# Performance work log

Measured on AMD Instinct MI355X. Metric: run time of the kernel, lower is better.

The kernel has to match this reference:

```python
import jax, jax.numpy as jnp
import numpy as np

N_EMBED = 1024
HEAD_SIZE = 128

def setup_inputs() -> dict:
    key = jax.random.key(0)
    kx, kq, kk, kv = jax.random.split(key, 4)
    B, T = 8, 2048
    x = jax.random.normal(kx, (B, T, N_EMBED), dtype=jnp.float32)
    s = 1.0 / np.sqrt(N_EMBED)
    Wq = jax.random.normal(kq, (N_EMBED, HEAD_SIZE), dtype=jnp.float32) * s
    Wk = jax.random.normal(kk, (N_EMBED, HEAD_SIZE), dtype=jnp.float32) * s
    Wv = jax.random.normal(kv, (N_EMBED, HEAD_SIZE), dtype=jnp.float32) * s
    return {"x": x, "Wq": Wq, "Wk": Wk, "Wv": Wv}

def reference(x, Wq, Wk, Wv):
    # x: [B, T, E]; single-head causal attention (nanoGPT-style Head)
    B, T, E = x.shape
    q = jnp.einsum('bte,eh->bth', x, Wq)  # [B,T,H]
    k = jnp.einsum('bte,eh->bth', x, Wk)
    v = jnp.einsum('bte,eh->bth', x, Wv)
    scale = 1.0 / jnp.sqrt(jnp.asarray(q.shape[-1], dtype=x.dtype))
    wei = jnp.einsum('bqh,bkh->bqk', q, k) * scale  # [B,T,T]
    causal = jnp.tril(jnp.ones((T, T), dtype=bool))
    wei = jnp.where(causal[None, :, :], wei, jnp.asarray(-jnp.inf, dtype=wei.dtype))
    attn = jax.nn.softmax(wei, axis=-1)
    out = jnp.einsum('bqk,bkh->bqh', attn, v)  # [B,T,H]
    return out
```

## Files before the change

### kernel.cpp

```cpp
#include <hip/hip_runtime.h>
#include <hip/hip_bf16.h>

typedef __bf16 bf16_t;
typedef bf16_t bf16x8 __attribute__((ext_vector_type(8)));
typedef bf16_t bf16x4 __attribute__((ext_vector_type(4)));
typedef float f32x4 __attribute__((ext_vector_type(4)));

#define MFMA16(a, b, c) __builtin_amdgcn_mfma_f32_16x16x32_bf16((a), (b), (c), 0, 0, 0)

#define TT 2048
#define EE 1024
#define HH 128
#define UPB 288


__global__ __launch_bounds__(256) void prep_w_kernel(
    const float* __restrict__ Wq, const float* __restrict__ Wk,
    const float* __restrict__ Wv, bf16_t* __restrict__ Wf)
{
    int idx = blockIdx.x * 256 + threadIdx.x;
    int e  = idx & 7;
    int c  = (idx >> 3) & 15;
    int g  = (idx >> 7) & 3;
    int kt = (idx >> 9) & 31;
    int ct = idx >> 14;
    int w  = ct >> 3;
    const float* W = (w == 0) ? Wq : (w == 1) ? Wk : Wv;
    int k = kt * 32 + g * 8 + e;
    int n = (ct & 7) * 16 + c;
    Wf[idx] = (bf16_t)W[k * HH + n];
}

__global__ __launch_bounds__(256) void qkv_kernel(
    const float* __restrict__ x, const bf16_t* __restrict__ Wf,
    bf16_t* __restrict__ Qf, bf16_t* __restrict__ Kf, bf16_t* __restrict__ Vf)
{
    __shared__ __attribute__((aligned(16))) bf16_t As[2][32][72];
    const int row0 = blockIdx.x * 32;
    const int tid  = threadIdx.x;
    const int lane = tid & 63;
    const int wn   = tid >> 6;
    const int g = lane >> 4, c = lane & 15;

    const int srow0 = tid >> 4;
    const int srow1 = 16 + srow0;
    const int scg   = (tid & 15) * 4;
    const float* xp0 = x + (size_t)(row0 + srow0) * EE + scg;
    const float* xp1 = x + (size_t)(row0 + srow1) * EE + scg;

    const bf16_t* wfbase = Wf + (size_t)wn * 6 * 32 * 512 + lane * 8;

    f32x4 acc[2][6];
    for (int i = 0; i < 2; ++i)
        for (int j = 0; j < 6; ++j) acc[i][j] = (f32x4)0.0f;

    f32x4 f0[2], f1[2];
    bf16x8 w[2][12];

#define BAR() do {                                                            \
    asm volatile("s_waitcnt lgkmcnt(0)" ::: "memory");                        \
    __builtin_amdgcn_s_barrier();                                             \
    __builtin_amdgcn_sched_barrier(0);                                        \
} while (0)
#define XLOAD(S, T) do {                                                      \
    f0[S] = *(const f32x4*)(xp0 + (size_t)(T) * 64);                          \
    f1[S] = *(const f32x4*)(xp1 + (size_t)(T) * 64);                          \
} while (0)
#define WLOAD(S, T) do {                                                      \
    for (int kk = 0; kk < 2; ++kk)                                            \
        for (int nt = 0; nt < 6; ++nt)                                        \
            w[S][kk * 6 + nt] = *(const bf16x8*)(wfbase +                     \
                ((size_t)nt * 32 + (T) * 2 + kk) * 512);                      \
} while (0)
#define XWRITE(S, BUF) do {                                                   \
    union { bf16_t h[4]; unsigned long long u; } p0_, p1_;                    \
    p0_.h[0] = (bf16_t)f0[S][0]; p0_.h[1] = (bf16_t)f0[S][1];                 \
    p0_.h[2] = (bf16_t)f0[S][2]; p0_.h[3] = (bf16_t)f0[S][3];                 \
    p1_.h[0] = (bf16_t)f1[S][0]; p1_.h[1] = (bf16_t)f1[S][1];                 \
    p1_.h[2] = (bf16_t)f1[S][2]; p1_.h[3] = (bf16_t)f1[S][3];                 \
    *reinterpret_cast<unsigned long long*>(&As[BUF][srow0][scg]) = p0_.u;     \
    *reinterpret_cast<unsigned long long*>(&As[BUF][srow1][scg]) = p1_.u;     \
} while (0)
#define PHASE(CUR, OTH, T) do {                                               \
    if ((T) + 2 < 16) XLOAD(CUR, (T) + 2);                                    \
    for (int kk = 0; kk < 2; ++kk)                                            \
        for (int mt = 0; mt < 2; ++mt) {                                      \
            bf16x8 af = *(const bf16x8*)&As[CUR][mt * 16 + c][kk * 32 + g * 8]; \
            for (int nt = 0; nt < 6; ++nt)                                    \
                acc[mt][nt] = MFMA16(af, w[CUR][kk * 6 + nt], acc[mt][nt]);   \
        }                                                                     \
    if ((T) + 2 < 16) WLOAD(CUR, (T) + 2);                                    \
    if ((T) + 1 < 16) XWRITE(OTH, OTH);                                       \
    BAR();                                                                    \
} while (0)

    XLOAD(0, 0);
    XLOAD(1, 1);
    WLOAD(0, 0);
    WLOAD(1, 1);
    XWRITE(0, 0);
    BAR();

    for (int tt = 0; tt < 16; tt += 2) {
        PHASE(0, 1, tt);
        PHASE(1, 0, tt + 1);
    }
#undef PHASE
#undef XLOAD
#undef WLOAD
#undef XWRITE
#undef BAR

    const float sc = 0.08838834764831845f * 1.4426950408889634f;
    for (int mt = 0; mt < 2; ++mt)
        for (int nt = 0; nt < 6; ++nt) {
            int cb = wn * 96 + nt * 16;
            int w_ = cb >> 7;
            int hl = (cb & 127) + c;
            int t0 = row0 + mt * 16 + g * 4;
            if (w_ == 2) {
                int b  = t0 >> 11;
                int ttr = t0 & (TT - 1);
                int vc = ttr >> 5, gg = (ttr & 31) >> 3, j0 = ttr & 7;
                int hb = hl >> 4, cc = hl & 15;
                union { bf16_t h4[4]; unsigned long long u; } pk;
                for (int i = 0; i < 4; ++i) pk.h4[i] = (bf16_t)acc[mt][nt][i];
                *reinterpret_cast<unsigned long long*>(
                    Vf + ((size_t)((b * 64 + vc) * 8 + hb)) * 512 +
                    (gg * 16 + cc) * 8 + j0) = pk.u;
            } else {
                bf16_t* dst = (w_ == 0) ? Qf : Kf;
                float s = (w_ == 0) ? sc : 1.0f;
                int kk = hl >> 5, gg = (hl & 31) >> 3, e = hl & 7;
                int grt = t0 >> 4;
                for (int i = 0; i < 4; ++i) {
                    int cr = (t0 + i) & 15;
                    dst[((size_t)(grt * 4 + kk)) * 512 + (gg * 16 + cr) * 8 + e] =
                        (bf16_t)(acc[mt][nt][i] * s);
                }
            }
        }
}

__global__ __launch_bounds__(256) void attn_kernel(
    const bf16_t* __restrict__ Qf, const bf16_t* __restrict__ Kf,
    const bf16_t* __restrict__ Vf, bf16_t* __restrict__ Pacc,
    float* __restrict__ Pml)
{
    __shared__ __attribute__((aligned(16))) bf16_t Pl[4][32][40];
    const int tid = threadIdx.x, lane = tid & 63, wid = tid >> 6;
    const int g = lane >> 4, c = lane & 15;
    bf16_t (*P)[40] = Pl[wid];

    const int bx = blockIdx.x;
    const int b  = bx & 7;
    const int u  = 287 - ((bx >> 3) * 4 + wid);
    int k = 0;
    while (4 * (k + 1) * (k + 2) <= u) ++k;
    const int r  = u - 4 * k * (k + 1);
    const int qt = 8 * k + r / (k + 1);
    const int ch = r - (r / (k + 1)) * (k + 1);
    const int q0 = qt * 32;
    const int kv_lo = ch * 256;
    int kv_hi = kv_lo + 256; if (kv_hi > q0 + 32) kv_hi = q0 + 32;
    const int sid = b * UPB + 4 * k * (k + 1) + (qt & 7) * (k + 1) + ch;

    bf16x8 qA[4], qB[4];
    for (int kk = 0; kk < 4; ++kk) {
        qA[kk] = *(const bf16x8*)(Qf +
            ((size_t)((b * 128 + (q0 >> 4)) * 4 + kk)) * 512 + lane * 8);
        qB[kk] = *(const bf16x8*)(Qf +
            ((size_t)((b * 128 + (q0 >> 4) + 1) * 4 + kk)) * 512 + lane * 8);
    }

    f32x4 accA[8], accB[8];
    for (int hb = 0; hb < 8; ++hb) { accA[hb] = (f32x4)0.0f; accB[hb] = (f32x4)0.0f; }
    float lsA[4] = {0, 0, 0, 0}, lsB[4] = {0, 0, 0, 0};

    for (int kv0 = kv_lo; kv0 < kv_hi; kv0 += 32) {
        const int kt = b * 128 + (kv0 >> 4);
        bf16x8 k0f[4], k1f[4], vf[8];
        for (int kk = 0; kk < 4; ++kk) {
            k0f[kk] = *(const bf16x8*)(Kf + ((size_t)(kt * 4 + kk)) * 512 + lane * 8);
            k1f[kk] = *(const bf16x8*)(Kf + ((size_t)((kt + 1) * 4 + kk)) * 512 + lane * 8);
        }
        const int vcb = (b * 64 + (kv0 >> 5)) * 8;
        for (int hb = 0; hb < 8; ++hb)
            vf[hb] = *(const bf16x8*)(Vf + ((size_t)(vcb + hb)) * 512 + lane * 8);

        f32x4 sA0 = (f32x4)0.0f, sA1 = (f32x4)0.0f;
        f32x4 sB0 = (f32x4)0.0f, sB1 = (f32x4)0.0f;
        for (int kk = 0; kk < 4; ++kk) {
            sA0 = MFMA16(qA[kk], k0f[kk], sA0);
            sA1 = MFMA16(qA[kk], k1f[kk], sA1);
            sB0 = MFMA16(qB[kk], k0f[kk], sB0);
            sB1 = MFMA16(qB[kk], k1f[kk], sB1);
        }
        if (kv0 + 32 > q0) {
            for (int i = 0; i < 4; ++i) {
                int row = q0 + g * 4 + i;
                if (kv0 + c > row)      sA0[i] = -1e30f;
                if (kv0 + 16 + c > row) sA1[i] = -1e30f;
            }
        }
        if (kv0 + 32 > q0 + 16) {
            for (int i = 0; i < 4; ++i) {
                int row = q0 + 16 + g * 4 + i;
                if (kv0 + c > row)      sB0[i] = -1e30f;
                if (kv0 + 16 + c > row) sB1[i] = -1e30f;
            }
        }
        float pA0[4], pA1[4], pB0[4], pB1[4];
        for (int i = 0; i < 4; ++i) {
            pA0[i] = exp2f(sA0[i]); pA1[i] = exp2f(sA1[i]);
            pB0[i] = exp2f(sB0[i]); pB1[i] = exp2f(sB1[i]);
            lsA[i] += pA0[i] + pA1[i];
            lsB[i] += pB0[i] + pB1[i];
        }
        for (int i = 0; i < 4; ++i) {
            P[g * 4 + i][c]           = (bf16_t)pA0[i];
            P[g * 4 + i][c + 16]      = (bf16_t)pA1[i];
            P[16 + g * 4 + i][c]      = (bf16_t)pB0[i];
            P[16 + g * 4 + i][c + 16] = (bf16_t)pB1[i];
        }
        __builtin_amdgcn_wave_barrier();
        asm volatile("s_waitcnt lgkmcnt(0)" ::: "memory");
        __builtin_amdgcn_sched_barrier(0);
        bf16x8 paA = *(const bf16x8*)&P[c][g * 8];
        bf16x8 paB = *(const bf16x8*)&P[16 + c][g * 8];
        __builtin_amdgcn_s_setprio(1);
        for (int hb = 0; hb < 8; ++hb) {
            accA[hb] = MFMA16(paA, vf[hb], accA[hb]);
            accB[hb] = MFMA16(paB, vf[hb], accB[hb]);
        }
        __builtin_amdgcn_s_setprio(0);
        __builtin_amdgcn_wave_barrier();
    }

    for (int off = 1; off < 16; off <<= 1)
        for (int i = 0; i < 4; ++i) {
            lsA[i] += __shfl_xor(lsA[i], off, 64);
            lsB[i] += __shfl_xor(lsB[i], off, 64);
        }
    if (c == 0)
        for (int i = 0; i < 4; ++i) {
            Pml[(size_t)sid * 32 + g * 4 + i]      = lsA[i];
            Pml[(size_t)sid * 32 + 16 + g * 4 + i] = lsB[i];
        }

    bf16_t* po = Pacc + (size_t)sid * (32 * 128);
    for (int hb = 0; hb < 8; ++hb) {
        union { bf16_t h4[4]; unsigned long long u; } pa, pb;
        for (int i = 0; i < 4; ++i) {
            pa.h4[i] = (bf16_t)accA[hb][i];
            pb.h4[i] = (bf16_t)accB[hb][i];
        }
        bf16_t* cp = po + (hb * 16 + c) * 32;
        *reinterpret_cast<unsigned long long*>(cp + g * 4)      = pa.u;
        *reinterpret_cast<unsigned long long*>(cp + 16 + g * 4) = pb.u;
    }
}

__global__ __launch_bounds__(128) void combine_kernel(
    const bf16_t* __restrict__ Pacc, const float* __restrict__ Pml,
    float* __restrict__ out)
{
    __shared__ float invL[32];
    const int qt = blockIdx.x;
    const int b  = blockIdx.y;
    const int k  = qt >> 3;
    const int base  = b * UPB + 4 * k * (k + 1) + (qt & 7) * (k + 1);
    const int count = k + 1;
    const int tid = threadIdx.x;

    if (tid < 32) {
        float L = 0.0f;
        for (int cu = 0; cu < count; ++cu)
            L += Pml[(size_t)(base + cu) * 32 + tid];
        invL[tid] = 1.0f / L;
    }
    __syncthreads();

    float s[32];
    for (int r = 0; r < 32; ++r) s[r] = 0.0f;
    for (int cu = 0; cu < count; ++cu) {
        const bf16_t* cp = Pacc + (size_t)(base + cu) * 4096 + tid * 32;
        for (int r8 = 0; r8 < 4; ++r8) {
            bf16x8 v = *(const bf16x8*)(cp + r8 * 8);
            for (int j = 0; j < 8; ++j) s[r8 * 8 + j] += (float)v[j];
        }
    }
    const int q0 = qt * 32;
    for (int r = 0; r < 32; ++r)
        out[((size_t)b * TT + q0 + r) * HH + tid] = s[r] * invL[r];
}

extern "C" void kernel_launch(void* const* d_in, const int* in_sizes, int n_in,
                              void* d_out, int out_size, void* d_ws, size_t ws_size,
                              hipStream_t stream)
{
    const float* x  = (const float*)d_in[0];
    const float* Wq = (const float*)d_in[1];
    const float* Wk = (const float*)d_in[2];
    const float* Wv = (const float*)d_in[3];

    char* ws = (char*)d_ws;
    bf16_t* Wf   = (bf16_t*)ws;
    bf16_t* Qf   = (bf16_t*)(ws + (1u  << 20));
    bf16_t* Kf   = (bf16_t*)(ws + (5u  << 20));
    bf16_t* Vf   = (bf16_t*)(ws + (9u  << 20));
    bf16_t* Pacc = (bf16_t*)(ws + (13u << 20));
    float*  Pml  = (float*) (ws + (32u << 20));

    prep_w_kernel<<<1536, 256, 0, stream>>>(Wq, Wk, Wv, Wf);
    qkv_kernel<<<512, 256, 0, stream>>>(x, Wf, Qf, Kf, Vf);
    attn_kernel<<<576, 256, 0, stream>>>(Qf, Kf, Vf, Pacc, Pml);
    combine_kernel<<<dim3(64, 8), 128, 0, stream>>>(Pacc, Pml, (float*)d_out);
}
```

Baseline: 68.32 us.

## Retile QKV projection to 64-row blocks split by N, and split combine across rows

The QKV GEMM now uses 64-row tiles with the 384 output columns split into two halves across the grid. Each wave computes 4x3 MFMA tiles instead of 2x6, and x loads are triple-buffered with wider per-thread vectors. MFMA sections run at raised priority via s_setprio. The combine kernel gains a z-dimension of 4 so each block handles 8 query rows, which gives more parallel blocks and fewer registers per thread. The cost is that each x tile is now read by two blocks.

```diff
diff --git a/kernel.cpp b/kernel.cpp
--- a/kernel.cpp
+++ b/kernel.cpp
@@ -35,86 +35,88 @@
     const float* __restrict__ x, const bf16_t* __restrict__ Wf,
     bf16_t* __restrict__ Qf, bf16_t* __restrict__ Kf, bf16_t* __restrict__ Vf)
 {
-    __shared__ __attribute__((aligned(16))) bf16_t As[2][32][72];
-    const int row0 = blockIdx.x * 32;
+    __shared__ __attribute__((aligned(16))) bf16_t As[2][64][72];
+    const int bx = blockIdx.x;
+    const int row0  = (bx & 255) * 64;
+    const int nhalf = bx >> 8;
     const int tid  = threadIdx.x;
     const int lane = tid & 63;
     const int wn   = tid >> 6;
     const int g = lane >> 4, c = lane & 15;
 
-    const int srow0 = tid >> 4;
-    const int srow1 = 16 + srow0;
-    const int scg   = (tid & 15) * 4;
-    const float* xp0 = x + (size_t)(row0 + srow0) * EE + scg;
-    const float* xp1 = x + (size_t)(row0 + srow1) * EE + scg;
-
-    const bf16_t* wfbase = Wf + (size_t)wn * 6 * 32 * 512 + lane * 8;
-
-    f32x4 acc[2][6];
-    for (int i = 0; i < 2; ++i)
-        for (int j = 0; j < 6; ++j) acc[i][j] = (f32x4)0.0f;
-
-    f32x4 f0[2], f1[2];
-    bf16x8 w[2][12];
+    const int srow = tid >> 2;
+    const int scg  = tid & 3;
+    const float* xp = x + (size_t)(row0 + srow) * EE + scg * 16;
+
+    const bf16_t* wfb = Wf + ((size_t)(nhalf * 12 + wn * 3) * 32) * 512 + lane * 8;
+
+    f32x4 acc[4][3];
+    for (int i = 0; i < 4; ++i)
+        for (int j = 0; j < 3; ++j) acc[i][j] = (f32x4)0.0f;
+
+    f32x4 xa[3][4];
+    bf16x8 w[2][6];
 
 #define BAR() do {                                                            \
     asm volatile("s_waitcnt lgkmcnt(0)" ::: "memory");                        \
     __builtin_amdgcn_s_barrier();                                             \
     __builtin_amdgcn_sched_barrier(0);                                        \
 } while (0)
-#define XLOAD(S, T) do {                                                      \
-    f0[S] = *(const f32x4*)(xp0 + (size_t)(T) * 64);                          \
-    f1[S] = *(const f32x4*)(xp1 + (size_t)(T) * 64);                          \
-} while (0)
-#define WLOAD(S, T) do {                                                      \
+#define XLOAD(S, T)                                                           \
+    for (int q = 0; q < 4; ++q)                                               \
+        xa[S][q] = *(const f32x4*)(xp + (size_t)(T) * 64 + q * 4);
+#define WLOAD(S, T)                                                           \
     for (int kk = 0; kk < 2; ++kk)                                            \
-        for (int nt = 0; nt < 6; ++nt)                                        \
-            w[S][kk * 6 + nt] = *(const bf16x8*)(wfbase +                     \
-                ((size_t)nt * 32 + (T) * 2 + kk) * 512);                      \
-} while (0)
+        for (int j = 0; j < 3; ++j)                                           \
+            w[S][kk * 3 + j] = *(const bf16x8*)(wfb +                         \
+                ((size_t)j * 32 + (T) * 2 + kk) * 512);
 #define XWRITE(S, BUF) do {                                                   \
-    union { bf16_t h[4]; unsigned long long u; } p0_, p1_;                    \
-    p0_.h[0] = (bf16_t)f0[S][0]; p0_.h[1] = (bf16_t)f0[S][1];                 \
-    p0_.h[2] = (bf16_t)f0[S][2]; p0_.h[3] = (bf16_t)f0[S][3];                 \
-    p1_.h[0] = (bf16_t)f1[S][0]; p1_.h[1] = (bf16_t)f1[S][1];                 \
-    p1_.h[2] = (bf16_t)f1[S][2]; p1_.h[3] = (bf16_t)f1[S][3];                 \
-    *reinterpret_cast<unsigned long long*>(&As[BUF][srow0][scg]) = p0_.u;     \
-    *reinterpret_cast<unsigned long long*>(&As[BUF][srow1][scg]) = p1_.u;     \
-} while (0)
-#define PHASE(CUR, OTH, T) do {                                               \
-    if ((T) + 2 < 16) XLOAD(CUR, (T) + 2);                                    \
-    for (int kk = 0; kk < 2; ++kk)                                            \
-        for (int mt = 0; mt < 2; ++mt) {                                      \
-            bf16x8 af = *(const bf16x8*)&As[CUR][mt * 16 + c][kk * 32 + g * 8]; \
-            for (int nt = 0; nt < 6; ++nt)                                    \
-                acc[mt][nt] = MFMA16(af, w[CUR][kk * 6 + nt], acc[mt][nt]);   \
-        }                                                                     \
-    if ((T) + 2 < 16) WLOAD(CUR, (T) + 2);                                    \
-    if ((T) + 1 < 16) XWRITE(OTH, OTH);                                       \
-    BAR();                                                                    \
+    union { bf16_t h[8]; unsigned long long u[2]; } pA_, pB_;                 \
+    for (int q = 0; q < 4; ++q) {                                             \
+        pA_.h[q]     = (bf16_t)xa[S][0][q];                                   \
+        pA_.h[4 + q] = (bf16_t)xa[S][1][q];                                   \
+        pB_.h[q]     = (bf16_t)xa[S][2][q];                                   \
+        pB_.h[4 + q] = (bf16_t)xa[S][3][q];                                   \
+    }                                                                         \
+    *reinterpret_cast<unsigned long long*>(&As[BUF][srow][scg * 16])     = pA_.u[0]; \
+    *reinterpret_cast<unsigned long long*>(&As[BUF][srow][scg * 16 + 4]) = pA_.u[1]; \
+    *reinterpret_cast<unsigned long long*>(&As[BUF][srow][scg * 16 + 8]) = pB_.u[0]; \
+    *reinterpret_cast<unsigned long long*>(&As[BUF][srow][scg * 16 +12]) = pB_.u[1]; \
 } while (0)
 
     XLOAD(0, 0);
     XLOAD(1, 1);
+    XLOAD(2, 2);
     WLOAD(0, 0);
     WLOAD(1, 1);
     XWRITE(0, 0);
     BAR();
 
-    for (int tt = 0; tt < 16; tt += 2) {
-        PHASE(0, 1, tt);
-        PHASE(1, 0, tt + 1);
-    }
-#undef PHASE
+#pragma unroll
+    for (int t = 0; t < 16; ++t) {
+        const int buf = t & 1;
+        if (t + 3 < 16) XLOAD((t + 3) % 3, t + 3);
+        __builtin_amdgcn_s_setprio(1);
+        for (int kk = 0; kk < 2; ++kk)
+            for (int mt = 0; mt < 4; ++mt) {
+                bf16x8 af = *(const bf16x8*)&As[buf][mt * 16 + c][kk * 32 + g * 8];
+                for (int j = 0; j < 3; ++j)
+                    acc[mt][j] = MFMA16(af, w[t & 1][kk * 3 + j], acc[mt][j]);
+            }
+        __builtin_amdgcn_s_setprio(0);
+        if (t + 2 < 16) WLOAD(t & 1, t + 2);
+        if (t + 1 < 16) XWRITE((t + 1) % 3, buf ^ 1);
+        BAR();
+    }
 #undef XLOAD
 #undef WLOAD
 #undef XWRITE
 #undef BAR
 
     const float sc = 0.08838834764831845f * 1.4426950408889634f;
-    for (int mt = 0; mt < 2; ++mt)
-        for (int nt = 0; nt < 6; ++nt) {
-            int cb = wn * 96 + nt * 16;
+    for (int mt = 0; mt < 4; ++mt)
+        for (int j = 0; j < 3; ++j) {
+            int cb = nhalf * 192 + wn * 48 + j * 16;
             int w_ = cb >> 7;
             int hl = (cb & 127) + c;
             int t0 = row0 + mt * 16 + g * 4;
@@ -124,7 +126,7 @@
                 int vc = ttr >> 5, gg = (ttr & 31) >> 3, j0 = ttr & 7;
                 int hb = hl >> 4, cc = hl & 15;
                 union { bf16_t h4[4]; unsigned long long u; } pk;
-                for (int i = 0; i < 4; ++i) pk.h4[i] = (bf16_t)acc[mt][nt][i];
+                for (int i = 0; i < 4; ++i) pk.h4[i] = (bf16_t)acc[mt][j][i];
                 *reinterpret_cast<unsigned long long*>(
                     Vf + ((size_t)((b * 64 + vc) * 8 + hb)) * 512 +
                     (gg * 16 + cc) * 8 + j0) = pk.u;
@@ -136,7 +138,7 @@
                 for (int i = 0; i < 4; ++i) {
                     int cr = (t0 + i) & 15;
                     dst[((size_t)(grt * 4 + kk)) * 512 + (gg * 16 + cr) * 8 + e] =
-                        (bf16_t)(acc[mt][nt][i] * s);
+                        (bf16_t)(acc[mt][j][i] * s);
                 }
             }
         }
@@ -265,33 +267,32 @@
     const bf16_t* __restrict__ Pacc, const float* __restrict__ Pml,
     float* __restrict__ out)
 {
-    __shared__ float invL[32];
+    __shared__ float invL[8];
     const int qt = blockIdx.x;
     const int b  = blockIdx.y;
+    const int qz = blockIdx.z;
     const int k  = qt >> 3;
     const int base  = b * UPB + 4 * k * (k + 1) + (qt & 7) * (k + 1);
     const int count = k + 1;
     const int tid = threadIdx.x;
 
-    if (tid < 32) {
+    if (tid < 8) {
         float L = 0.0f;
         for (int cu = 0; cu < count; ++cu)
-            L += Pml[(size_t)(base + cu) * 32 + tid];
+            L += Pml[(size_t)(base + cu) * 32 + qz * 8 + tid];
         invL[tid] = 1.0f / L;
     }
     __syncthreads();
 
-    float s[32];
-    for (int r = 0; r < 32; ++r) s[r] = 0.0f;
+    float s[8];
+    for (int r = 0; r < 8; ++r) s[r] = 0.0f;
     for (int cu = 0; cu < count; ++cu) {
-        const bf16_t* cp = Pacc + (size_t)(base + cu) * 4096 + tid * 32;
-        for (int r8 = 0; r8 < 4; ++r8) {
-            bf16x8 v = *(const bf16x8*)(cp + r8 * 8);
-            for (int j = 0; j < 8; ++j) s[r8 * 8 + j] += (float)v[j];
-        }
-    }
-    const int q0 = qt * 32;
-    for (int r = 0; r < 32; ++r)
+        bf16x8 v = *(const bf16x8*)(
+            Pacc + (size_t)(base + cu) * 4096 + tid * 32 + qz * 8);
+        for (int j = 0; j < 8; ++j) s[j] += (float)v[j];
+    }
+    const int q0 = qt * 32 + qz * 8;
+    for (int r = 0; r < 8; ++r)
         out[((size_t)b * TT + q0 + r) * HH + tid] = s[r] * invL[r];
 }
 
@@ -315,5 +316,5 @@
     prep_w_kernel<<<1536, 256, 0, stream>>>(Wq, Wk, Wv, Wf);
     qkv_kernel<<<512, 256, 0, stream>>>(x, Wf, Qf, Kf, Vf);
     attn_kernel<<<576, 256, 0, stream>>>(Qf, Kf, Vf, Pacc, Pml);
-    combine_kernel<<<dim3(64, 8), 128, 0, stream>>>(Pacc, Pml, (float*)d_out);
-}
+    combine_kernel<<<dim3(64, 8, 4), 128, 0, stream>>>(Pacc, Pml, (float*)d_out);
+}
```

Measured after the change: 66.63 us. 1.03x faster.
